# Kernel optimization log

Measured on AMD Instinct MI355X. Metric: run time of the kernel, lower is better.

The kernel has to match this reference:

```python
import jax, jax.numpy as jnp
import numpy as np

DIM = 1024
NUM_HEADS = 16
HEAD_DIM = DIM // NUM_HEADS


def setup_inputs() -> dict:
    key = jax.random.key(0)
    ks = jax.random.split(key, 9)
    s = 1.0 / np.sqrt(DIM)
    return {
        "x": jax.random.normal(ks[0], (2, 2048, DIM), dtype=jnp.float32),
        "wq": jax.random.uniform(ks[1], (DIM, DIM), jnp.float32, -s, s),
        "bq": jax.random.uniform(ks[2], (DIM,), jnp.float32, -s, s),
        "wk": jax.random.uniform(ks[3], (DIM, DIM), jnp.float32, -s, s),
        "bk": jax.random.uniform(ks[4], (DIM,), jnp.float32, -s, s),
        "wv": jax.random.uniform(ks[5], (DIM, DIM), jnp.float32, -s, s),
        "bv": jax.random.uniform(ks[6], (DIM,), jnp.float32, -s, s),
        "wo": jax.random.uniform(ks[7], (DIM, DIM), jnp.float32, -s, s),
        "bo": jax.random.uniform(ks[8], (DIM,), jnp.float32, -s, s),
    }


def reference(x, wq, bq, wk, bk, wv, bv, wo, bo):
    B, N, D = x.shape
    H, Hd = NUM_HEADS, HEAD_DIM
    # projections; weights stored as (in, out) so x @ w matches torch Linear(x) with w = W.T
    q = (x @ wq + bq).reshape(B, N, H, Hd).transpose(0, 2, 1, 3)  # [B,H,N,Hd]
    k = (x @ wk + bk).reshape(B, N, H, Hd).transpose(0, 2, 1, 3)
    v = (x @ wv + bv).reshape(B, N, H, Hd).transpose(0, 2, 1, 3)
    scale = 1.0 / np.sqrt(Hd).astype(np.float32)
    scores = jnp.einsum("bhqd,bhkd->bhqk", q, k) * scale  # [B,H,N,N]
    attn = jax.nn.softmax(scores, axis=-1)
    # dropout is identity in eval mode (reference baseline)
    out = jnp.einsum("bhqk,bhkd->bhqd", attn, v)  # [B,H,N,Hd]
    out = out.transpose(0, 2, 1, 3).reshape(B, N, D)
    return out @ wo + bo
```

## Files before the change

### kernel.cpp

```cpp
#include <hip/hip_runtime.h>

typedef __attribute__((ext_vector_type(8))) short short8;
typedef __attribute__((ext_vector_type(4))) short short4v;
typedef __attribute__((ext_vector_type(4))) float f32x4;

__device__ inline unsigned short f2bf(float f) {
  union { float f; unsigned int u; } v; v.f = f;
  unsigned int r = v.u + 0x7FFFu + ((v.u >> 16) & 1u);
  return (unsigned short)(r >> 16);
}

__device__ inline unsigned cvtpk_bf16(float lo, float hi) {
  unsigned r;
  asm("v_cvt_pk_bf16_f32 %0, %1, %2" : "=v"(r) : "v"(lo), "v"(hi));
  return r;
}

__device__ inline void gload_lds16(const void* g, void* l) {
  __builtin_amdgcn_global_load_lds(
      (const __attribute__((address_space(1))) unsigned int*)g,
      (__attribute__((address_space(3))) unsigned int*)l, 16, 0, 0);
}


__global__ __launch_bounds__(256) void prep(
    const float* __restrict__ x,
    const float* __restrict__ wq, const float* __restrict__ wk,
    const float* __restrict__ wv, const float* __restrict__ wo,
    const float* __restrict__ bq, const float* __restrict__ bk,
    const float* __restrict__ bv,
    unsigned short* __restrict__ xb, unsigned short* __restrict__ wqkvT,
    unsigned short* __restrict__ woT, float* __restrict__ bqkv) {
  const int bid = blockIdx.x;
  if (bid < 4096) {
    const int i = bid * 256 + threadIdx.x;
    float4 v = ((const float4*)x)[i];
    ushort4 o;
    o.x = f2bf(v.x); o.y = f2bf(v.y); o.z = f2bf(v.z); o.w = f2bf(v.w);
    ((ushort4*)xb)[i] = o;
  } else if (bid < 8192) {
    const int u = bid - 4096;
    const int z = u >> 10, rem = u & 1023;
    const float* w = (z == 0) ? wq : (z == 1) ? wk : (z == 2) ? wv : wo;
    unsigned short* dst = (z < 3) ? (wqkvT + (size_t)z * 1024 * 1024) : woT;
    const float scale = (z == 0) ? 0.18033688011f : 1.0f;
    __shared__ float t[32][33];
    const int k0 = (rem & 31) * 32;
    const int n0 = (rem >> 5) * 32;
    const int tx = threadIdx.x & 31, ty = threadIdx.x >> 5;
#pragma unroll
    for (int i = 0; i < 32; i += 8)
      t[ty + i][tx] = w[(size_t)(k0 + ty + i) * 1024 + n0 + tx];
    __syncthreads();
#pragma unroll
    for (int i = 0; i < 32; i += 8)
      dst[(size_t)(n0 + ty + i) * 1024 + k0 + tx] = f2bf(t[tx][ty + i] * scale);
  } else {
    const int i = (bid - 8192) * 256 + threadIdx.x;
    float v;
    if (i < 1024) v = bq[i] * 0.18033688011f;
    else if (i < 2048) v = bk[i - 1024];
    else v = bv[i - 2048];
    bqkv[i] = v;
  }
}


__global__ __launch_bounds__(256) void gemm_bt64(
    const unsigned short* __restrict__ A, const unsigned short* __restrict__ Bt,
    const float* __restrict__ bias, float* __restrict__ C, int K, int ldc) {
  __shared__ unsigned short As[64 * 32];
  __shared__ unsigned short Bs[128 * 32];
  const int tid = threadIdx.x;
  const int lane = tid & 63;
  const int wave = tid >> 6;
  const int wm = (wave >> 1) * 32;
  const int wn = (wave & 1) * 64;
  const long bm = (long)blockIdx.x * 64;
  const long bn = (long)blockIdx.y * 128;

  const int sr = tid >> 2;
  const int sc = (tid & 3) * 8;
  const unsigned short* Ag0 = A + (bm + sr) * (long)K + sc;
  const unsigned short* Bg0 = Bt + (bn + sr) * (long)K + sc;
  const unsigned short* Bg1 = Bt + (bn + 64 + sr) * (long)K + sc;
  unsigned short* As0 = &As[tid * 8];
  unsigned short* Bs0 = &Bs[tid * 8];
  unsigned short* Bs1 = &Bs[2048 + tid * 8];

  f32x4 acc[2][4] = {};

  const int fr = lane & 15;
  const int fk = (lane >> 4) * 8;

  for (int kt = 0; kt < K; kt += 32) {
    gload_lds16(Ag0, As0);
    gload_lds16(Bg0, Bs0);
    gload_lds16(Bg1, Bs1);
    Ag0 += 32; Bg0 += 32; Bg1 += 32;
    __syncthreads();
    short8 af[2], bfv[4];
#pragma unroll
    for (int i = 0; i < 2; i++) af[i] = *(const short8*)&As[(wm + i * 16 + fr) * 32 + fk];
#pragma unroll
    for (int j = 0; j < 4; j++) bfv[j] = *(const short8*)&Bs[(wn + j * 16 + fr) * 32 + fk];
#pragma unroll
    for (int i = 0; i < 2; i++)
#pragma unroll
      for (int j = 0; j < 4; j++)
        acc[i][j] = __builtin_amdgcn_mfma_f32_16x16x32_bf16(af[i], bfv[j], acc[i][j], 0, 0, 0);
    __syncthreads();
  }

  const int crow = (lane >> 4) * 4;
  const int ccol = lane & 15;
#pragma unroll
  for (int j = 0; j < 4; j++) {
    const long col = bn + wn + j * 16 + ccol;
    const float bv = bias[col];
#pragma unroll
    for (int i = 0; i < 2; i++)
#pragma unroll
      for (int r = 0; r < 4; r++) {
        const long row = bm + wm + i * 16 + crow + r;
        C[row * ldc + col] = acc[i][j][r] + bv;
      }
  }
}


__global__ __launch_bounds__(512, 2) void gemm256(
    const unsigned short* __restrict__ A, const unsigned short* __restrict__ Bt,
    const float* __restrict__ bias, unsigned short* __restrict__ C, int ldc) {
  constexpr int K = 1024;
  __shared__ unsigned short Sab[2][2][16384];
  const int tid = threadIdx.x;
  const int lane = tid & 63;
  const int w = tid >> 6;
  const int wr = w >> 2, wc = w & 3;
  const long bm = (long)blockIdx.x * 256;
  const long bn = (long)blockIdx.y * 256;
  const int fr = lane & 15, fg = lane >> 4;

  const int srow = tid >> 3;
  const int kch = tid & 7;

  auto stage = [&](int o, int buf, int tk, int h) {
#pragma unroll
    for (int l = 0; l < 2; ++l) {
      const int rih = l * 64 + srow;
      const unsigned short* src = (o ? Bt : A) +
          ((o ? bn : bm) + h * 128 + rih) * (long)K + tk * 64 + ((kch ^ (rih & 7)) * 8);
      gload_lds16(src, &Sab[buf][o][h * 8192 + (l * 512 + tid) * 8]);
    }
  };

  f32x4 acc[8][4] = {};

  stage(0, 0, 0, 0); stage(0, 0, 0, 1);
  stage(1, 0, 0, 0); stage(1, 0, 0, 1);
  stage(1, 1, 1, 0); stage(1, 1, 1, 1);
  asm volatile("s_waitcnt vmcnt(4)" ::: "memory");
  __builtin_amdgcn_s_barrier();

  for (int it = 0; it < 8; ++it) {
    const int T = 2 * it;
    const int tkA = (T + 2 < 15) ? T + 2 : 15;
    const int tkB3 = (T + 3 < 15) ? T + 3 : 15;
#pragma unroll
    for (int half = 0; half < 2; ++half) {
      const int b = half;
      short8 bfr[4][2];
      short8 afr[2][2];
#pragma unroll
      for (int g = 0; g < 4; ++g) {
        if (g == 0) {
#pragma unroll
          for (int nj = 0; nj < 4; ++nj)
#pragma unroll
            for (int kc = 0; kc < 2; ++kc) {
              const int r = wc * 64 + nj * 16 + fr;
              bfr[nj][kc] = *(const short8*)&Sab[b][1][r * 64 + ((kc * 4 + fg) ^ (r & 7)) * 8];
            }
        }
#pragma unroll
        for (int mil = 0; mil < 2; ++mil)
#pragma unroll
          for (int kc = 0; kc < 2; ++kc) {
            const int r = wr * 128 + (2 * g + mil) * 16 + fr;
            afr[mil][kc] = *(const short8*)&Sab[b][0][r * 64 + ((kc * 4 + fg) ^ (r & 7)) * 8];
          }
        if (half == 0) {
          if (g == 0)      { stage(0, 1, T + 1, 0); stage(0, 1, T + 1, 1); }
          else if (g == 1) { stage(1, 0, tkA, 0); }
          else if (g == 2) { stage(1, 0, tkA, 1); }
        } else {
          if (g == 0)      { stage(0, 0, tkA, 0); stage(0, 0, tkA, 1); }
          else if (g == 1) { stage(1, 1, tkB3, 0); }
          else if (g == 2) { stage(1, 1, tkB3, 1); }
        }
        __builtin_amdgcn_s_barrier();
        asm volatile("s_waitcnt lgkmcnt(0)" ::: "memory");
        __builtin_amdgcn_sched_barrier(0);
        __builtin_amdgcn_s_setprio(1);
#pragma unroll
        for (int mil = 0; mil < 2; ++mil)
#pragma unroll
          for (int nj = 0; nj < 4; ++nj)
#pragma unroll
            for (int kc = 0; kc < 2; ++kc)
              acc[2 * g + mil][nj] = __builtin_amdgcn_mfma_f32_16x16x32_bf16(
                  afr[mil][kc], bfr[nj][kc], acc[2 * g + mil][nj], 0, 0, 0);
        __builtin_amdgcn_s_setprio(0);
        if (g == 3) asm volatile("s_waitcnt vmcnt(4)" ::: "memory");
        __builtin_amdgcn_s_barrier();
      }
    }
  }

  const int crow = fg * 4;
  const int ccol = fr;
#pragma unroll
  for (int nj = 0; nj < 4; ++nj) {
    const long col = bn + wc * 64 + nj * 16 + ccol;
    const float bv = bias[col];
#pragma unroll
    for (int mi = 0; mi < 8; ++mi)
#pragma unroll
      for (int r = 0; r < 4; ++r) {
        const long row = bm + wr * 128 + mi * 16 + crow + r;
        C[row * ldc + col] = f2bf(acc[mi][nj][r] + bv);
      }
  }
}


#define KSWZ(row) (((row) & 3) | ((((row) >> 3) & 1) << 2))
#define TRRD(d, o) asm volatile("ds_read_b64_tr_b16 %0, %1 offset:" o \
                                : "=v"(d) : "v"(vtr) : "memory")
#define LGKM(n) asm volatile("s_waitcnt lgkmcnt(" #n ")" ::: "memory")

__global__ __launch_bounds__(512, 4) void attn_fwd(
    const unsigned short* __restrict__ qkv, unsigned short* __restrict__ out) {
  __shared__ unsigned short S[4 * 4096];
  __shared__ float msArr[512];
  unsigned short* Ks = &S[0];
  unsigned short* Vs = &S[8192];
  const int tid = threadIdx.x;
  const int lane = tid & 63;
  const int w = tid >> 6;
  const int qh = w >> 1, kh = w & 1;

  const int xcd = blockIdx.x & 7, slot = blockIdx.x >> 3;
  const int pair = xcd * 4 + (slot >> 4);
  const int qtile = slot & 15;
  const int h = pair & 15, b = pair >> 4;
  const long rowbase = (long)b * 2048;
  const int hq = h * 64;
  const int fr = lane & 15;
  const int fg = lane >> 4;
  const int fk = fg * 8;
  const int q0 = qtile * 128 + qh * 32;

  short8 qf[2][2];
#pragma unroll
  for (int qi = 0; qi < 2; qi++) {
    const long qr = rowbase + q0 + qi * 16 + fr;
    qf[qi][0] = *(const short8*)&qkv[qr * 3072 + hq + fk];
    qf[qi][1] = *(const short8*)&qkv[qr * 3072 + hq + 32 + fk];
  }

  const int kr = tid >> 3;
  const unsigned short* Kg = &qkv[(rowbase + kr) * 3072 + 1024 + hq + (((tid & 7) ^ KSWZ(kr)) * 8)];
  const int vkv = ((tid >> 1) & 3) + ((tid >> 5) & 1) * 4 + ((tid >> 3) & 3) * 8 + ((tid >> 8) & 1) * 32;
  const int vd0 = (tid & 1) * 8 + ((tid >> 6) & 3) * 16;
  const unsigned short* Vg = &qkv[(rowbase + vkv) * 3072 + 2048 + hq + vd0];

  auto stage = [&](int buf) {
    gload_lds16(Kg, &Ks[buf * 4096 + tid * 8]);
    gload_lds16(Vg, &Vs[buf * 4096 + tid * 8]);
    Kg += 64 * 3072; Vg += 64 * 3072;
  };

  f32x4 o[2][4] = {};
  float m_[2] = {-1e30f, -1e30f};
  float s_[2] = {0.f, 0.f};

  const int krowbase = kh * 32 + (fr >> 2) * 8 + (fr & 3);

  stage(0);
  __syncthreads();

  for (int t = 0; t < 32; t++) {
    const int cur = t & 1;
    if (t < 31) stage(cur ^ 1);

    f32x4 sa[2][2];
    __builtin_amdgcn_s_setprio(1);
#pragma unroll
    for (int n = 0; n < 2; n++) {
      const int row = krowbase + n * 4;
      const short8 kf0 = *(const short8*)&Ks[cur * 4096 + ((row * 64 + fk) ^ (KSWZ(row) << 3))];
      const short8 kf1 = *(const short8*)&Ks[cur * 4096 + ((row * 64 + 32 + fk) ^ (KSWZ(row) << 3))];
#pragma unroll
      for (int qi = 0; qi < 2; qi++) {
        f32x4 z = {0.f, 0.f, 0.f, 0.f};
        z = __builtin_amdgcn_mfma_f32_16x16x32_bf16(kf0, qf[qi][0], z, 0, 0, 0);
        sa[qi][n] = __builtin_amdgcn_mfma_f32_16x16x32_bf16(kf1, qf[qi][1], z, 0, 0, 0);
      }
    }
    __builtin_amdgcn_s_setprio(0);

    float lmax[2];
#pragma unroll
    for (int qi = 0; qi < 2; qi++)
      lmax[qi] = fmaxf(fmaxf(fmaxf(sa[qi][0][0], sa[qi][0][1]), fmaxf(sa[qi][0][2], sa[qi][0][3])),
                       fmaxf(fmaxf(sa[qi][1][0], sa[qi][1][1]), fmaxf(sa[qi][1][2], sa[qi][1][3])));
    if (__any(fmaxf(lmax[0] - m_[0], lmax[1] - m_[1]) > 8.f)) {
#pragma unroll
      for (int qi = 0; qi < 2; qi++) {
        float mx = lmax[qi];
        mx = fmaxf(mx, __shfl_xor(mx, 16));
        mx = fmaxf(mx, __shfl_xor(mx, 32));
        const float nm = fmaxf(m_[qi], mx);
        const float fac = __builtin_amdgcn_exp2f(m_[qi] - nm);
        m_[qi] = nm;
        s_[qi] *= fac;
        float facp[4];
#pragma unroll
        for (int r = 0; r < 4; r++) facp[r] = __shfl(fac, fg * 4 + r);
#pragma unroll
        for (int dj = 0; dj < 4; dj++)
#pragma unroll
          for (int r = 0; r < 4; r++) o[qi][dj][r] *= facp[r];
      }
    }

    short8 pa[2];
#pragma unroll
    for (int qi = 0; qi < 2; qi++) {
      float p[8];
#pragma unroll
      for (int n = 0; n < 2; n++)
#pragma unroll
        for (int r = 0; r < 4; r++)
          p[n * 4 + r] = __builtin_amdgcn_exp2f(sa[qi][n][r] - m_[qi]);
      float sl = ((p[0] + p[1]) + (p[2] + p[3])) + ((p[4] + p[5]) + (p[6] + p[7]));
      sl += __shfl_xor(sl, 16);
      sl += __shfl_xor(sl, 32);
      s_[qi] += sl;
      union { unsigned u[4]; short8 v; } pk;
      pk.u[0] = cvtpk_bf16(p[0], p[1]);
      pk.u[1] = cvtpk_bf16(p[2], p[3]);
      pk.u[2] = cvtpk_bf16(p[4], p[5]);
      pk.u[3] = cvtpk_bf16(p[6], p[7]);
      pa[qi] = pk.v;
    }

    const __attribute__((address_space(3))) unsigned short* vtr =
        (const __attribute__((address_space(3))) unsigned short*)&Vs[0] +
        cur * 4096 + kh * 2048 + lane * 4;
    short4v v0[4], v1[4];
    TRRD(v0[0], "0");    TRRD(v1[0], "512");
    TRRD(v0[1], "1024"); TRRD(v1[1], "1536");
    TRRD(v0[2], "2048"); TRRD(v1[2], "2560");
    TRRD(v0[3], "3072"); TRRD(v1[3], "3584");

    __builtin_amdgcn_s_setprio(1);
    LGKM(6); __builtin_amdgcn_sched_barrier(0);
    {
      short8 vf = __builtin_shufflevector(v0[0], v1[0], 0, 1, 2, 3, 4, 5, 6, 7);
      o[0][0] = __builtin_amdgcn_mfma_f32_16x16x32_bf16(pa[0], vf, o[0][0], 0, 0, 0);
      o[1][0] = __builtin_amdgcn_mfma_f32_16x16x32_bf16(pa[1], vf, o[1][0], 0, 0, 0);
    }
    LGKM(4); __builtin_amdgcn_sched_barrier(0);
    {
      short8 vf = __builtin_shufflevector(v0[1], v1[1], 0, 1, 2, 3, 4, 5, 6, 7);
      o[0][1] = __builtin_amdgcn_mfma_f32_16x16x32_bf16(pa[0], vf, o[0][1], 0, 0, 0);
      o[1][1] = __builtin_amdgcn_mfma_f32_16x16x32_bf16(pa[1], vf, o[1][1], 0, 0, 0);
    }
    LGKM(2); __builtin_amdgcn_sched_barrier(0);
    {
      short8 vf = __builtin_shufflevector(v0[2], v1[2], 0, 1, 2, 3, 4, 5, 6, 7);
      o[0][2] = __builtin_amdgcn_mfma_f32_16x16x32_bf16(pa[0], vf, o[0][2], 0, 0, 0);
      o[1][2] = __builtin_amdgcn_mfma_f32_16x16x32_bf16(pa[1], vf, o[1][2], 0, 0, 0);
    }
    LGKM(0); __builtin_amdgcn_sched_barrier(0);
    {
      short8 vf = __builtin_shufflevector(v0[3], v1[3], 0, 1, 2, 3, 4, 5, 6, 7);
      o[0][3] = __builtin_amdgcn_mfma_f32_16x16x32_bf16(pa[0], vf, o[0][3], 0, 0, 0);
      o[1][3] = __builtin_amdgcn_mfma_f32_16x16x32_bf16(pa[1], vf, o[1][3], 0, 0, 0);
    }
    __builtin_amdgcn_s_setprio(0);
    __syncthreads();
  }

  float* mo = (float*)&S[0];
  __syncthreads();
  if (kh == 1) {
#pragma unroll
    for (int qi = 0; qi < 2; qi++)
#pragma unroll
      for (int dj = 0; dj < 4; dj++)
#pragma unroll
        for (int r = 0; r < 4; r++)
          mo[(qh * 32 + qi * 16 + dj * 4 + r) * 64 + lane] = o[qi][dj][r];
  }
  if (fg == 0) {
#pragma unroll
    for (int qi = 0; qi < 2; qi++) {
      msArr[(((kh * 4 + qh) * 2 + qi) * 2 + 0) * 16 + fr] = m_[qi];
      msArr[(((kh * 4 + qh) * 2 + qi) * 2 + 1) * 16 + fr] = s_[qi];
    }
  }
  __syncthreads();
  if (kh == 0) {
#pragma unroll
    for (int qi = 0; qi < 2; qi++) {
      float f0[4], f1[4], rs[4];
#pragma unroll
      for (int r = 0; r < 4; r++) {
        const int qp = fg * 4 + r;
        const float m0 = msArr[(((0 * 4 + qh) * 2 + qi) * 2 + 0) * 16 + qp];
        const float s0 = msArr[(((0 * 4 + qh) * 2 + qi) * 2 + 1) * 16 + qp];
        const float m1 = msArr[(((1 * 4 + qh) * 2 + qi) * 2 + 0) * 16 + qp];
        const float s1 = msArr[(((1 * 4 + qh) * 2 + qi) * 2 + 1) * 16 + qp];
        const float mstar = fmaxf(m0, m1);
        f0[r] = __builtin_amdgcn_exp2f(m0 - mstar);
        f1[r] = __builtin_amdgcn_exp2f(m1 - mstar);
        rs[r] = __builtin_amdgcn_rcpf(s0 * f0[r] + s1 * f1[r]);
      }
#pragma unroll
      for (int dj = 0; dj < 4; dj++)
#pragma unroll
        for (int r = 0; r < 4; r++) {
          const float o1 = mo[(qh * 32 + qi * 16 + dj * 4 + r) * 64 + lane];
          const float val = (o[qi][dj][r] * f0[r] + o1 * f1[r]) * rs[r];
          const long row = rowbase + q0 + qi * 16 + fg * 4 + r;
          out[row * 1024 + hq + dj * 16 + fr] = f2bf(val);
        }
    }
  }
}


extern "C" void kernel_launch(void* const* d_in, const int* in_sizes, int n_in,
                              void* d_out, int out_size, void* d_ws, size_t ws_size,
                              hipStream_t stream) {
  const float* x  = (const float*)d_in[0];
  const float* wq = (const float*)d_in[1];
  const float* bq = (const float*)d_in[2];
  const float* wk = (const float*)d_in[3];
  const float* bk = (const float*)d_in[4];
  const float* wv = (const float*)d_in[5];
  const float* bv = (const float*)d_in[6];
  const float* wo = (const float*)d_in[7];
  const float* bo = (const float*)d_in[8];

  char* ws = (char*)d_ws;
  unsigned short* xb    = (unsigned short*)(ws);
  unsigned short* wqkvT = (unsigned short*)(ws + (8ull  << 20));
  unsigned short* woT   = (unsigned short*)(ws + (14ull << 20));
  float*          bqkv  = (float*)         (ws + (16ull << 20));
  unsigned short* qkv   = (unsigned short*)(ws + (17ull << 20));
  unsigned short* attn  = (unsigned short*)(ws + (41ull << 20));

  prep<<<8204, 256, 0, stream>>>(x, wq, wk, wv, wo, bq, bk, bv, xb, wqkvT, woT, bqkv);

  gemm256<<<dim3(16, 12), 512, 0, stream>>>(xb, wqkvT, bqkv, qkv, 3072);

  attn_fwd<<<512, 512, 0, stream>>>(qkv, attn);

  gemm_bt64<<<dim3(64, 8), 256, 0, stream>>>(attn, woT, bo, (float*)d_out, 1024, 1024);
}
```

Baseline: 118.0 us.

## Software-pipeline PV matmul one tile behind with triple-buffered V

The attention loop now runs the P·V MFMAs for the previous KV tile right after the QK^T MFMAs of the current tile. This overlaps the matrix work with the softmax exponentials, and a final PV step is peeled out after the loop. V gets a third LDS buffer so the tile being read, the current tile and the tile being prefetched never collide. The cost is more shared memory per block (S grows from 4 to 5 × 4096 shorts), which may reduce how many blocks fit per CU at the requested launch bound, plus some extra registers to carry `pa` across iterations.

```diff
diff --git a/kernel.cpp b/kernel.cpp
--- a/kernel.cpp
+++ b/kernel.cpp
@@ -242,7 +242,7 @@
 
 __global__ __launch_bounds__(512, 4) void attn_fwd(
     const unsigned short* __restrict__ qkv, unsigned short* __restrict__ out) {
-  __shared__ unsigned short S[4 * 4096];
+  __shared__ unsigned short S[5 * 4096];
   __shared__ float msArr[512];
   unsigned short* Ks = &S[0];
   unsigned short* Vs = &S[8192];
@@ -276,32 +276,36 @@
   const int vd0 = (tid & 1) * 8 + ((tid >> 6) & 3) * 16;
   const unsigned short* Vg = &qkv[(rowbase + vkv) * 3072 + 2048 + hq + vd0];
 
-  auto stage = [&](int buf) {
-    gload_lds16(Kg, &Ks[buf * 4096 + tid * 8]);
-    gload_lds16(Vg, &Vs[buf * 4096 + tid * 8]);
+  auto stage = [&](int kbuf, int vbuf) {
+    gload_lds16(Kg, &Ks[kbuf * 4096 + tid * 8]);
+    gload_lds16(Vg, &Vs[vbuf * 4096 + tid * 8]);
     Kg += 64 * 3072; Vg += 64 * 3072;
   };
 
   f32x4 o[2][4] = {};
   float m_[2] = {-1e30f, -1e30f};
   float s_[2] = {0.f, 0.f};
+  short8 pa[2] = {};
 
   const int krowbase = kh * 32 + (fr >> 2) * 8 + (fr & 3);
 
-  stage(0);
+  stage(0, 0);
   __syncthreads();
 
+  int vcur = 0, vprev = 0;
+
   for (int t = 0; t < 32; t++) {
-    const int cur = t & 1;
-    if (t < 31) stage(cur ^ 1);
+    const int kcur = t & 1;
+    const int vnxt = (vcur == 2) ? 0 : vcur + 1;
+    if (t < 31) stage((t + 1) & 1, vnxt);
 
     f32x4 sa[2][2];
     __builtin_amdgcn_s_setprio(1);
 #pragma unroll
     for (int n = 0; n < 2; n++) {
       const int row = krowbase + n * 4;
-      const short8 kf0 = *(const short8*)&Ks[cur * 4096 + ((row * 64 + fk) ^ (KSWZ(row) << 3))];
-      const short8 kf1 = *(const short8*)&Ks[cur * 4096 + ((row * 64 + 32 + fk) ^ (KSWZ(row) << 3))];
+      const short8 kf0 = *(const short8*)&Ks[kcur * 4096 + ((row * 64 + fk) ^ (KSWZ(row) << 3))];
+      const short8 kf1 = *(const short8*)&Ks[kcur * 4096 + ((row * 64 + 32 + fk) ^ (KSWZ(row) << 3))];
 #pragma unroll
       for (int qi = 0; qi < 2; qi++) {
         f32x4 z = {0.f, 0.f, 0.f, 0.f};
@@ -311,11 +315,32 @@
     }
     __builtin_amdgcn_s_setprio(0);
 
+    const __attribute__((address_space(3))) unsigned short* vtr =
+        (const __attribute__((address_space(3))) unsigned short*)&Vs[0] +
+        vprev * 4096 + kh * 2048 + lane * 4;
+    short4v v0[4], v1[4];
+    TRRD(v0[0], "0");    TRRD(v1[0], "512");
+    TRRD(v0[1], "1024"); TRRD(v1[1], "1536");
+    TRRD(v0[2], "2048"); TRRD(v1[2], "2560");
+    TRRD(v0[3], "3072"); TRRD(v1[3], "3584");
+
     float lmax[2];
 #pragma unroll
     for (int qi = 0; qi < 2; qi++)
       lmax[qi] = fmaxf(fmaxf(fmaxf(sa[qi][0][0], sa[qi][0][1]), fmaxf(sa[qi][0][2], sa[qi][0][3])),
                        fmaxf(fmaxf(sa[qi][1][0], sa[qi][1][1]), fmaxf(sa[qi][1][2], sa[qi][1][3])));
+
+    LGKM(0);
+    __builtin_amdgcn_sched_barrier(0);
+    __builtin_amdgcn_s_setprio(1);
+#pragma unroll
+    for (int dj = 0; dj < 4; dj++) {
+      short8 vf = __builtin_shufflevector(v0[dj], v1[dj], 0, 1, 2, 3, 4, 5, 6, 7);
+      o[0][dj] = __builtin_amdgcn_mfma_f32_16x16x32_bf16(pa[0], vf, o[0][dj], 0, 0, 0);
+      o[1][dj] = __builtin_amdgcn_mfma_f32_16x16x32_bf16(pa[1], vf, o[1][dj], 0, 0, 0);
+    }
+    __builtin_amdgcn_s_setprio(0);
+
     if (__any(fmaxf(lmax[0] - m_[0], lmax[1] - m_[1]) > 8.f)) {
 #pragma unroll
       for (int qi = 0; qi < 2; qi++) {
@@ -336,7 +361,6 @@
       }
     }
 
-    short8 pa[2];
 #pragma unroll
     for (int qi = 0; qi < 2; qi++) {
       float p[8];
@@ -357,42 +381,28 @@
       pa[qi] = pk.v;
     }
 
+    vprev = vcur;
+    vcur = vnxt;
+    __syncthreads();
+  }
+
+  {
     const __attribute__((address_space(3))) unsigned short* vtr =
         (const __attribute__((address_space(3))) unsigned short*)&Vs[0] +
-        cur * 4096 + kh * 2048 + lane * 4;
+        vprev * 4096 + kh * 2048 + lane * 4;
     short4v v0[4], v1[4];
     TRRD(v0[0], "0");    TRRD(v1[0], "512");
     TRRD(v0[1], "1024"); TRRD(v1[1], "1536");
     TRRD(v0[2], "2048"); TRRD(v1[2], "2560");
     TRRD(v0[3], "3072"); TRRD(v1[3], "3584");
-
-    __builtin_amdgcn_s_setprio(1);
-    LGKM(6); __builtin_amdgcn_sched_barrier(0);
-    {
-      short8 vf = __builtin_shufflevector(v0[0], v1[0], 0, 1, 2, 3, 4, 5, 6, 7);
-      o[0][0] = __builtin_amdgcn_mfma_f32_16x16x32_bf16(pa[0], vf, o[0][0], 0, 0, 0);
-      o[1][0] = __builtin_amdgcn_mfma_f32_16x16x32_bf16(pa[1], vf, o[1][0], 0, 0, 0);
-    }
-    LGKM(4); __builtin_amdgcn_sched_barrier(0);
-    {
-      short8 vf = __builtin_shufflevector(v0[1], v1[1], 0, 1, 2, 3, 4, 5, 6, 7);
-      o[0][1] = __builtin_amdgcn_mfma_f32_16x16x32_bf16(pa[0], vf, o[0][1], 0, 0, 0);
-      o[1][1] = __builtin_amdgcn_mfma_f32_16x16x32_bf16(pa[1], vf, o[1][1], 0, 0, 0);
-    }
-    LGKM(2); __builtin_amdgcn_sched_barrier(0);
-    {
-      short8 vf = __builtin_shufflevector(v0[2], v1[2], 0, 1, 2, 3, 4, 5, 6, 7);
-      o[0][2] = __builtin_amdgcn_mfma_f32_16x16x32_bf16(pa[0], vf, o[0][2], 0, 0, 0);
-      o[1][2] = __builtin_amdgcn_mfma_f32_16x16x32_bf16(pa[1], vf, o[1][2], 0, 0, 0);
-    }
-    LGKM(0); __builtin_amdgcn_sched_barrier(0);
-    {
-      short8 vf = __builtin_shufflevector(v0[3], v1[3], 0, 1, 2, 3, 4, 5, 6, 7);
-      o[0][3] = __builtin_amdgcn_mfma_f32_16x16x32_bf16(pa[0], vf, o[0][3], 0, 0, 0);
-      o[1][3] = __builtin_amdgcn_mfma_f32_16x16x32_bf16(pa[1], vf, o[1][3], 0, 0, 0);
-    }
-    __builtin_amdgcn_s_setprio(0);
-    __syncthreads();
+    LGKM(0);
+    __builtin_amdgcn_sched_barrier(0);
+#pragma unroll
+    for (int dj = 0; dj < 4; dj++) {
+      short8 vf = __builtin_shufflevector(v0[dj], v1[dj], 0, 1, 2, 3, 4, 5, 6, 7);
+      o[0][dj] = __builtin_amdgcn_mfma_f32_16x16x32_bf16(pa[0], vf, o[0][dj], 0, 0, 0);
+      o[1][dj] = __builtin_amdgcn_mfma_f32_16x16x32_bf16(pa[1], vf, o[1][dj], 0, 0, 0);
+    }
   }
 
   float* mo = (float*)&S[0];
```

New measurement: 127.3 us. +7.9%, slower.

## Triple-buffer K/V tiles in attention with prefetch distance two

Applied to the files above, without the earlier changes.

Grows the K/V shared-memory staging from two to three buffers and issues loads two tiles ahead. Each iteration waits only until the older load group has landed (vmcnt(2)) before the barrier, so more memory latency is hidden behind compute. Shared memory per block rises and the occupancy hint drops from 4 to 2 blocks per CU. Near the end the same final tile is loaded redundantly to keep the wait counts uniform.

```diff
diff --git a/kernel.cpp b/kernel.cpp
--- a/kernel.cpp
+++ b/kernel.cpp
@@ -240,12 +240,12 @@
                                 : "=v"(d) : "v"(vtr) : "memory")
 #define LGKM(n) asm volatile("s_waitcnt lgkmcnt(" #n ")" ::: "memory")
 
-__global__ __launch_bounds__(512, 4) void attn_fwd(
+__global__ __launch_bounds__(512, 2) void attn_fwd(
     const unsigned short* __restrict__ qkv, unsigned short* __restrict__ out) {
-  __shared__ unsigned short S[4 * 4096];
+  __shared__ unsigned short S[6 * 4096];
   __shared__ float msArr[512];
   unsigned short* Ks = &S[0];
-  unsigned short* Vs = &S[8192];
+  unsigned short* Vs = &S[3 * 4096];
   const int tid = threadIdx.x;
   const int lane = tid & 63;
   const int w = tid >> 6;
@@ -271,15 +271,15 @@
   }
 
   const int kr = tid >> 3;
-  const unsigned short* Kg = &qkv[(rowbase + kr) * 3072 + 1024 + hq + (((tid & 7) ^ KSWZ(kr)) * 8)];
+  const unsigned short* Kg0 = &qkv[(rowbase + kr) * 3072 + 1024 + hq + (((tid & 7) ^ KSWZ(kr)) * 8)];
   const int vkv = ((tid >> 1) & 3) + ((tid >> 5) & 1) * 4 + ((tid >> 3) & 3) * 8 + ((tid >> 8) & 1) * 32;
   const int vd0 = (tid & 1) * 8 + ((tid >> 6) & 3) * 16;
-  const unsigned short* Vg = &qkv[(rowbase + vkv) * 3072 + 2048 + hq + vd0];
-
-  auto stage = [&](int buf) {
-    gload_lds16(Kg, &Ks[buf * 4096 + tid * 8]);
-    gload_lds16(Vg, &Vs[buf * 4096 + tid * 8]);
-    Kg += 64 * 3072; Vg += 64 * 3072;
+  const unsigned short* Vg0 = &qkv[(rowbase + vkv) * 3072 + 2048 + hq + vd0];
+
+  auto stage = [&](int tk, int buf) {
+    const long off = (long)tk * 64 * 3072;
+    gload_lds16(Kg0 + off, &Ks[buf * 4096 + tid * 8]);
+    gload_lds16(Vg0 + off, &Vs[buf * 4096 + tid * 8]);
   };
 
   f32x4 o[2][4] = {};
@@ -288,12 +288,19 @@
 
   const int krowbase = kh * 32 + (fr >> 2) * 8 + (fr & 3);
 
-  stage(0);
-  __syncthreads();
+  stage(0, 0);
+  stage(1, 1);
+  asm volatile("s_waitcnt vmcnt(2)" ::: "memory");
+  __builtin_amdgcn_s_barrier();
+
+  int cur = 0;
 
   for (int t = 0; t < 32; t++) {
-    const int cur = t & 1;
-    if (t < 31) stage(cur ^ 1);
+    {
+      int stg = cur + 2; if (stg >= 3) stg -= 3;
+      const int tk = (t + 2 < 31) ? t + 2 : 31;
+      stage(tk, stg);
+    }
 
     f32x4 sa[2][2];
     __builtin_amdgcn_s_setprio(1);
@@ -392,7 +399,11 @@
       o[1][3] = __builtin_amdgcn_mfma_f32_16x16x32_bf16(pa[1], vf, o[1][3], 0, 0, 0);
     }
     __builtin_amdgcn_s_setprio(0);
-    __syncthreads();
+
+    asm volatile("s_waitcnt vmcnt(2) lgkmcnt(0)" ::: "memory");
+    __builtin_amdgcn_s_barrier();
+
+    cur = (cur == 2) ? 0 : cur + 1;
   }
 
   float* mo = (float*)&S[0];
```

Measured after the change: 117.7 us. About the same (-0.3%).

## Split attention KV range across two blocks and merge partials in separate kernel

Applied to the files above, without the earlier changes.

Splits each attention query tile's key/value sequence into two halves handled by separate blocks, doubling the grid to 1024 blocks. Each block writes unnormalized fp32 partial outputs plus per-row max and sum to workspace, and a new merge kernel combines the halves and writes the bf16 result. This is meant to fill more CUs (512 blocks on a 256-CU part gives a single wave) and shorten each block's serial loop. In exchange it adds fp32 partial traffic (about 32MB written and read back) and an extra kernel launch. Launch bounds are also raised to 8 waves per SIMD.

```diff
diff --git a/kernel.cpp b/kernel.cpp
--- a/kernel.cpp
+++ b/kernel.cpp
@@ -240,8 +240,9 @@
                                 : "=v"(d) : "v"(vtr) : "memory")
 #define LGKM(n) asm volatile("s_waitcnt lgkmcnt(" #n ")" ::: "memory")
 
-__global__ __launch_bounds__(512, 4) void attn_fwd(
-    const unsigned short* __restrict__ qkv, unsigned short* __restrict__ out) {
+__global__ __launch_bounds__(512, 8) void attn_fwd(
+    const unsigned short* __restrict__ qkv, float* __restrict__ po,
+    float* __restrict__ msb) {
   __shared__ unsigned short S[4 * 4096];
   __shared__ float msArr[512];
   unsigned short* Ks = &S[0];
@@ -252,10 +253,13 @@
   const int qh = w >> 1, kh = w & 1;
 
   const int xcd = blockIdx.x & 7, slot = blockIdx.x >> 3;
-  const int pair = xcd * 4 + (slot >> 4);
-  const int qtile = slot & 15;
+  const int pair = xcd * 4 + (slot >> 5);
+  const int rem = slot & 31;
+  const int qtile = rem >> 1;
+  const int kvs = rem & 1;
   const int h = pair & 15, b = pair >> 4;
   const long rowbase = (long)b * 2048;
+  const long kvbase = rowbase + (long)kvs * 1024;
   const int hq = h * 64;
   const int fr = lane & 15;
   const int fg = lane >> 4;
@@ -271,10 +275,10 @@
   }
 
   const int kr = tid >> 3;
-  const unsigned short* Kg = &qkv[(rowbase + kr) * 3072 + 1024 + hq + (((tid & 7) ^ KSWZ(kr)) * 8)];
+  const unsigned short* Kg = &qkv[(kvbase + kr) * 3072 + 1024 + hq + (((tid & 7) ^ KSWZ(kr)) * 8)];
   const int vkv = ((tid >> 1) & 3) + ((tid >> 5) & 1) * 4 + ((tid >> 3) & 3) * 8 + ((tid >> 8) & 1) * 32;
   const int vd0 = (tid & 1) * 8 + ((tid >> 6) & 3) * 16;
-  const unsigned short* Vg = &qkv[(rowbase + vkv) * 3072 + 2048 + hq + vd0];
+  const unsigned short* Vg = &qkv[(kvbase + vkv) * 3072 + 2048 + hq + vd0];
 
   auto stage = [&](int buf) {
     gload_lds16(Kg, &Ks[buf * 4096 + tid * 8]);
@@ -291,9 +295,9 @@
   stage(0);
   __syncthreads();
 
-  for (int t = 0; t < 32; t++) {
+  for (int t = 0; t < 16; t++) {
     const int cur = t & 1;
-    if (t < 31) stage(cur ^ 1);
+    if (t < 15) stage(cur ^ 1);
 
     f32x4 sa[2][2];
     __builtin_amdgcn_s_setprio(1);
@@ -417,7 +421,7 @@
   if (kh == 0) {
 #pragma unroll
     for (int qi = 0; qi < 2; qi++) {
-      float f0[4], f1[4], rs[4];
+      float f0[4], f1[4], mst[4], st[4];
 #pragma unroll
       for (int r = 0; r < 4; r++) {
         const int qp = fg * 4 + r;
@@ -425,22 +429,56 @@
         const float s0 = msArr[(((0 * 4 + qh) * 2 + qi) * 2 + 1) * 16 + qp];
         const float m1 = msArr[(((1 * 4 + qh) * 2 + qi) * 2 + 0) * 16 + qp];
         const float s1 = msArr[(((1 * 4 + qh) * 2 + qi) * 2 + 1) * 16 + qp];
-        const float mstar = fmaxf(m0, m1);
-        f0[r] = __builtin_amdgcn_exp2f(m0 - mstar);
-        f1[r] = __builtin_amdgcn_exp2f(m1 - mstar);
-        rs[r] = __builtin_amdgcn_rcpf(s0 * f0[r] + s1 * f1[r]);
+        mst[r] = fmaxf(m0, m1);
+        f0[r] = __builtin_amdgcn_exp2f(m0 - mst[r]);
+        f1[r] = __builtin_amdgcn_exp2f(m1 - mst[r]);
+        st[r] = s0 * f0[r] + s1 * f1[r];
       }
 #pragma unroll
       for (int dj = 0; dj < 4; dj++)
 #pragma unroll
         for (int r = 0; r < 4; r++) {
           const float o1 = mo[(qh * 32 + qi * 16 + dj * 4 + r) * 64 + lane];
-          const float val = (o[qi][dj][r] * f0[r] + o1 * f1[r]) * rs[r];
+          const float val = o[qi][dj][r] * f0[r] + o1 * f1[r];
           const long row = rowbase + q0 + qi * 16 + fg * 4 + r;
-          out[row * 1024 + hq + dj * 16 + fr] = f2bf(val);
+          po[((long)kvs * 4096 + row) * 1024 + hq + dj * 16 + fr] = val;
         }
-    }
-  }
+      if (fr == 0) {
+#pragma unroll
+        for (int r = 0; r < 4; r++) {
+          const long row = rowbase + q0 + qi * 16 + fg * 4 + r;
+          msb[(((long)kvs * 4096 + row) * 16 + h) * 2 + 0] = mst[r];
+          msb[(((long)kvs * 4096 + row) * 16 + h) * 2 + 1] = st[r];
+        }
+      }
+    }
+  }
+}
+
+
+__global__ __launch_bounds__(256) void attn_merge(
+    const float4* __restrict__ po4, const float* __restrict__ msb,
+    ushort4* __restrict__ outv) {
+  const long idx = (long)blockIdx.x * 256 + threadIdx.x;
+  const long row = idx >> 8;
+  const int q4 = (int)(idx & 255);
+  const int head = q4 >> 4;
+  float4 a = po4[row * 256 + q4];
+  float4 c = po4[(4096 + row) * 256 + q4];
+  const float ma = msb[(row * 16 + head) * 2 + 0];
+  const float sa = msb[(row * 16 + head) * 2 + 1];
+  const float mb = msb[((4096 + row) * 16 + head) * 2 + 0];
+  const float sb = msb[((4096 + row) * 16 + head) * 2 + 1];
+  const float mst = fmaxf(ma, mb);
+  const float fa = __builtin_amdgcn_exp2f(ma - mst);
+  const float fb = __builtin_amdgcn_exp2f(mb - mst);
+  const float rs = __builtin_amdgcn_rcpf(sa * fa + sb * fb);
+  ushort4 o;
+  o.x = f2bf((a.x * fa + c.x * fb) * rs);
+  o.y = f2bf((a.y * fa + c.y * fb) * rs);
+  o.z = f2bf((a.z * fa + c.z * fb) * rs);
+  o.w = f2bf((a.w * fa + c.w * fb) * rs);
+  outv[idx] = o;
 }
 
 
@@ -464,12 +502,15 @@
   float*          bqkv  = (float*)         (ws + (16ull << 20));
   unsigned short* qkv   = (unsigned short*)(ws + (17ull << 20));
   unsigned short* attn  = (unsigned short*)(ws + (41ull << 20));
+  float*          po    = (float*)         (ws + (50ull << 20));
+  float*          msb   = (float*)         (ws + (82ull << 20));
 
   prep<<<8204, 256, 0, stream>>>(x, wq, wk, wv, wo, bq, bk, bv, xb, wqkvT, woT, bqkv);
 
   gemm256<<<dim3(16, 12), 512, 0, stream>>>(xb, wqkvT, bqkv, qkv, 3072);
 
-  attn_fwd<<<512, 512, 0, stream>>>(qkv, attn);
+  attn_fwd<<<1024, 512, 0, stream>>>(qkv, po, msb);
+  attn_merge<<<4096, 256, 0, stream>>>((const float4*)po, msb, (ushort4*)attn);
 
   gemm_bt64<<<dim3(64, 8), 256, 0, stream>>>(attn, woT, bo, (float*)d_out, 1024, 1024);
 }
```

After: 344.2 us. +191.6%, slower.
